# Kernel tuning notes

Hardware: AMD Instinct MI355X
Metric: run time of the kernel (lower is better)

The kernel has to match this reference:

```python
import jax, jax.numpy as jnp
import numpy as np
from jax import lax


def _conv(x, w, b):
    # NCHW valid conv, stride 1 (torch Conv2d semantics)
    y = lax.conv_general_dilated(x, w, (1, 1), 'VALID',
                                 dimension_numbers=('NCHW', 'OIHW', 'NCHW'))
    return y + b[None, :, None, None]


def _maxpool(x, k, s):
    return lax.reduce_window(x, -jnp.inf, lax.max, (1, 1, k, k), (1, 1, s, s), 'VALID')


def _lin(x, w, b):
    # torch nn.Linear: y = x @ W^T + b, applied to last dim
    return x @ w.T + b


def setup_inputs() -> dict:
    key = jax.random.key(0)
    ks = jax.random.split(key, 21)
    def f(i, shape, scale):
        return jax.random.normal(ks[i], shape, dtype=jnp.float32) * scale
    return {
        'x': f(0, (512, 1, 28, 28), 1.0),
        'c1_w': f(1, (50, 1, 3, 3), 0.33), 'c1_b': f(2, (50,), 0.1),
        'c2_w': f(3, (50, 50, 3, 3), 0.047), 'c2_b': f(4, (50,), 0.05),
        'c3_w': f(5, (50, 50, 3, 3), 0.047), 'c3_b': f(6, (50,), 0.05),
        'l1_w': f(7, (500, 50), 0.14), 'l1_b': f(8, (500,), 0.05),
        'l2_w': f(9, (10, 500), 0.045), 'l2_b': f(10, (10,), 0.05),
        'd1_w': f(11, (3, 8450), 0.011), 'd1_b': f(12, (3,), 0.05),
        'd2_w': f(13, (2, 1250), 0.028), 'd2_b': f(14, (2,), 0.05),
        'c1c3_w': f(15, (13, 13), 0.28), 'c1c3_b': f(16, (13,), 0.05),
        'c1l1_w': f(17, (500, 1), 1.0), 'c1l1_b': f(18, (500,), 0.05),
        'c2l1_w': f(19, (500, 5), 0.45), 'c2l1_b': f(20, (500,), 0.05),
    }


def reference(x, c1_w, c1_b, c2_w, c2_b, c3_w, c3_b, l1_w, l1_b, l2_w, l2_b,
              d1_w, d1_b, d2_w, d2_b, c1c3_w, c1c3_b, c1l1_w, c1l1_b,
              c2l1_w, c2l1_b):
    B = x.shape[0]
    # stage 1: conv1 + relu + pool2 -> [B,50,13,13]
    h1 = _maxpool(jax.nn.relu(_conv(x, c1_w, c1_b)), 2, 2)
    # router 1 (argmax over 3 branches): 0 -> conv2 path, 1 -> c1_c3 path, 2 -> early-exit linear path
    d1 = jnp.argmax(_lin(h1.reshape(B, -1), d1_w, d1_b), axis=1)  # [B]
    # branch l11 (d1==2): pool7 -> [B,50,1,1], Linear(1->500) on last dim -> [B,50,1,500]
    l11 = _lin(_maxpool(h1, 7, 7), c1l1_w, c1l1_b)
    # branch c3-direct (d1==1): Linear(13->13) on last dim, then conv3+relu+pool2 -> [B,50,5,5]
    c33 = _lin(h1, c1c3_w, c1c3_b)
    c3d = _maxpool(jax.nn.relu(_conv(c33, c3_w, c3_b)), 2, 2)
    # branch c2 (d1==0): conv2+relu+pool2 -> [B,50,5,5]
    h2 = _maxpool(jax.nn.relu(_conv(h1, c2_w, c2_b)), 2, 2)
    # router 2 (argmax over 2 sub-branches)
    d2 = jnp.argmax(_lin(h2.reshape(B, -1), d2_w, d2_b), axis=1)  # [B]
    # sub-branch c32 (d2==0): conv3+relu+pool2 -> [B,50,1,1]
    c32 = _maxpool(jax.nn.relu(_conv(h2, c3_w, c3_b)), 2, 2)
    # sub-branch l12 (d2==1): Linear(5->500) on last dim -> [B,50,5,500], pool3 -> [B,50,1,166]
    l12 = _maxpool(_lin(h2, c2l1_w, c2l1_b), 3, 3)

    def head(t):
        # original: .view(-1, 50) -> linear1/relu/linear2/log_softmax; row-major flatten per sample
        r = t.reshape(B, -1, 50)
        return jax.nn.log_softmax(_lin(jax.nn.relu(_lin(r, l1_w, l1_b)), l2_w, l2_b), axis=-1)

    dt = x.dtype
    m_l11 = (d1 == 2).astype(dt)[:, None, None]
    m_c3d = (d1 == 1).astype(dt)[:, None, None]
    m_c32 = ((d1 == 0) & (d2 == 0)).astype(dt)[:, None, None]
    m_l12 = ((d1 == 0) & (d2 == 1)).astype(dt)[:, None, None]
    # dense masked combine (static-shape equivalent of the gather/compute/concat dispatch);
    # branch order matches the original concatenation: l11, l12, c32, c3-direct
    out = jnp.concatenate([head(l11) * m_l11, head(l12) * m_l12,
                           head(c32) * m_c32, head(c3d) * m_c3d], axis=1)  # [B,692,10]
    return out, d1, d2
```

## Files before the change

### kernel.cpp

```cpp
#include <hip/hip_runtime.h>
#include <hip/hip_bf16.h>
#include <math.h>

#define BB 512
#define CC 50

typedef __attribute__((ext_vector_type(8))) __bf16 bf16x8;
typedef __attribute__((ext_vector_type(4))) float f32x4;

__global__ void k_zero(float* __restrict__ out, int n4) {
  int i = blockIdx.x * 256 + threadIdx.x;
  if (i < n4) {
    float4 z = {0.f, 0.f, 0.f, 0.f};
    ((float4*)out)[i] = z;
  }
}

__global__ void k_pack(const float* __restrict__ l1w, const float* __restrict__ l1b,
                       const float* __restrict__ l2w,
                       __bf16* __restrict__ W1p, float* __restrict__ W2t) {
  int idx = blockIdx.x * 256 + threadIdx.x;
  if (idx < 512 * 64) {
    int j = idx >> 6, k = idx & 63;
    float v = 0.f;
    if (j < 500) {
      if (k < 50) v = l1w[j * 50 + k];
      else if (k == 50) v = l1b[j];
    }
    W1p[idx] = (__bf16)v;
  } else if (idx < 512 * 64 + 512 * 12) {
    int i2 = idx - 512 * 64;
    int j = i2 / 12, n = i2 % 12;
    W2t[i2] = (n < 10 && j < 500) ? l2w[n * 500 + j] : 0.f;
  }
}

__global__ void k_conv1(const float* __restrict__ x, const float* __restrict__ w,
                        const float* __restrict__ bias, float* __restrict__ h1) {
  int idx = blockIdx.x * 256 + threadIdx.x;
  if (idx >= BB * CC * 169) return;
  int b = idx / (CC * 169);
  int rem = idx % (CC * 169);
  int c = rem / 169;
  int p = rem % 169;
  int py = p / 13, px = p % 13;
  const float* xi = x + b * 784;
  float wr[9];
#pragma unroll
  for (int i = 0; i < 9; i++) wr[i] = w[c * 9 + i];
  float m = -INFINITY;
#pragma unroll
  for (int dy = 0; dy < 2; dy++)
#pragma unroll
    for (int dx = 0; dx < 2; dx++) {
      int y0 = 2 * py + dy, x0 = 2 * px + dx;
      float s = 0.f;
#pragma unroll
      for (int ky = 0; ky < 3; ky++)
#pragma unroll
        for (int kx = 0; kx < 3; kx++)
          s += xi[(y0 + ky) * 28 + x0 + kx] * wr[ky * 3 + kx];
      m = fmaxf(m, s);
    }
  h1[idx] = fmaxf(m + bias[c], 0.f);
}

__global__ void k_d1p7(const float* __restrict__ h1, const float* __restrict__ w,
                       const float* __restrict__ bias, int* __restrict__ d1i,
                       float* __restrict__ outd1, float* __restrict__ p7) {
  int b = blockIdx.x, t = threadIdx.x;
  const float* hb = h1 + b * 8450;
  float s0 = 0.f, s1 = 0.f, s2 = 0.f;
  for (int i = t; i < 8450; i += 256) {
    float v = hb[i];
    s0 += v * w[i];
    s1 += v * w[8450 + i];
    s2 += v * w[16900 + i];
  }
#pragma unroll
  for (int off = 32; off >= 1; off >>= 1) {
    s0 += __shfl_down(s0, off);
    s1 += __shfl_down(s1, off);
    s2 += __shfl_down(s2, off);
  }
  __shared__ float red[4][3];
  if ((t & 63) == 0) { red[t >> 6][0] = s0; red[t >> 6][1] = s1; red[t >> 6][2] = s2; }
  __syncthreads();
  if (t == 0) {
    float l0 = bias[0], l1v = bias[1], l2v = bias[2];
    for (int wv = 0; wv < 4; wv++) { l0 += red[wv][0]; l1v += red[wv][1]; l2v += red[wv][2]; }
    int idx = 0; float best = l0;
    if (l1v > best) { best = l1v; idx = 1; }
    if (l2v > best) { best = l2v; idx = 2; }
    d1i[b] = idx;
    outd1[b] = (float)idx;
  }
  if (t < 50) {
    const float* hp = hb + t * 169;
    float m = -INFINITY;
#pragma unroll
    for (int y = 0; y < 7; y++)
#pragma unroll
      for (int x = 0; x < 7; x++) m = fmaxf(m, hp[y * 13 + x]);
    p7[b * 50 + t] = m;
  }
}

__global__ __launch_bounds__(256) void k_conv5m(
    const float* __restrict__ h1,
    const float* __restrict__ c2w, const float* __restrict__ c2b,
    const float* __restrict__ c3w, const float* __restrict__ c3b,
    const int* __restrict__ d1i,
    const float* __restrict__ w13, const float* __restrict__ b13,
    float* __restrict__ h2, float* __restrict__ c3d) {
  int id = blockIdx.x;
  int mode = id & 1, b = id >> 1;
  if (mode == 1 && d1i[b] != 1) return;
  __shared__ float sh[50 * 260];
  __shared__ float w13s[182];
  int t = threadIdx.x;
  for (int i = t; i < 8450; i += 256) {
    int ic = i / 169, r = i % 169;
    sh[ic * 260 + (r / 13) * 20 + (r % 13)] = h1[b * 8450 + i];
  }
  if (mode == 1) {
    for (int i = t; i < 182; i += 256) w13s[i] = (i < 169) ? w13[i] : b13[i - 169];
  }
  __syncthreads();
  if (mode == 1) {
    for (int p = t; p < 650; p += 256) {
      float* row = sh + (p / 13) * 260 + (p % 13) * 20;
      float r[13];
#pragma unroll
      for (int k = 0; k < 13; k++) r[k] = row[k];
#pragma unroll
      for (int xx = 0; xx < 13; xx++) {
        float s = w13s[169 + xx];
#pragma unroll
        for (int k = 0; k < 13; k++) s += r[k] * w13s[xx * 13 + k];
        row[xx] = s;
      }
    }
    __syncthreads();
  }
  if (t >= 250) return;
  int oc = t / 5, py = t % 5;
  const float* wb = (mode ? c3w : c2w) + oc * 450;
  float acc[5][4];
#pragma unroll
  for (int i = 0; i < 5; i++)
#pragma unroll
    for (int j = 0; j < 4; j++) acc[i][j] = 0.f;
  for (int ic = 0; ic < 50; ic++) {
    float wv[9];
#pragma unroll
    for (int i = 0; i < 9; i++) wv[i] = wb[ic * 9 + i];
    float r[4][13];
    const float* rp = sh + ic * 260 + 2 * py * 20;
#pragma unroll
    for (int rr = 0; rr < 4; rr++) {
      const float* p4 = rp + rr * 20;
      float4 q0 = *(const float4*)(p4);
      float4 q1 = *(const float4*)(p4 + 4);
      float4 q2 = *(const float4*)(p4 + 8);
      r[rr][0] = q0.x; r[rr][1] = q0.y; r[rr][2] = q0.z; r[rr][3] = q0.w;
      r[rr][4] = q1.x; r[rr][5] = q1.y; r[rr][6] = q1.z; r[rr][7] = q1.w;
      r[rr][8] = q2.x; r[rr][9] = q2.y; r[rr][10] = q2.z; r[rr][11] = q2.w;
      r[rr][12] = p4[12];
    }
#pragma unroll
    for (int px = 0; px < 5; px++)
#pragma unroll
      for (int dy = 0; dy < 2; dy++)
#pragma unroll
        for (int dx = 0; dx < 2; dx++) {
          float s = acc[px][dy * 2 + dx];
          int x0 = 2 * px + dx;
#pragma unroll
          for (int ky = 0; ky < 3; ky++)
#pragma unroll
            for (int kx = 0; kx < 3; kx++)
              s += r[dy + ky][x0 + kx] * wv[ky * 3 + kx];
          acc[px][dy * 2 + dx] = s;
        }
  }
  float bs = (mode ? c3b : c2b)[oc];
  float* outp = mode ? c3d : h2;
#pragma unroll
  for (int px = 0; px < 5; px++) {
    float m = fmaxf(fmaxf(acc[px][0], acc[px][1]), fmaxf(acc[px][2], acc[px][3]));
    outp[(b * 50 + oc) * 25 + py * 5 + px] = fmaxf(m + bs, 0.f);
  }
}

__global__ __launch_bounds__(256) void k_d2c(const float* __restrict__ h2,
                                             const float* __restrict__ d2w,
                                             const float* __restrict__ d2b,
                                             const float* __restrict__ c3w,
                                             const float* __restrict__ c3b,
                                             const float* __restrict__ c2l1w,
                                             const float* __restrict__ c2l1b,
                                             const int* __restrict__ d1i,
                                             int* __restrict__ d2i,
                                             float* __restrict__ outd2,
                                             float* __restrict__ c32,
                                             float* __restrict__ l12) {
  int b = blockIdx.x, t = threadIdx.x;
  __shared__ float hs[1250];
  __shared__ float wls[2500];
  __shared__ float bls[500];
  __shared__ float red[4][2];
  __shared__ int sd2;
  for (int i = t; i < 1250; i += 256) hs[i] = h2[b * 1250 + i];
  __syncthreads();
  float s0 = 0.f, s1 = 0.f;
  for (int i = t; i < 1250; i += 256) {
    float v = hs[i];
    s0 += v * d2w[i];
    s1 += v * d2w[1250 + i];
  }
#pragma unroll
  for (int off = 32; off >= 1; off >>= 1) {
    s0 += __shfl_down(s0, off);
    s1 += __shfl_down(s1, off);
  }
  if ((t & 63) == 0) { red[t >> 6][0] = s0; red[t >> 6][1] = s1; }
  __syncthreads();
  if (t == 0) {
    float l0 = d2b[0] + red[0][0] + red[1][0] + red[2][0] + red[3][0];
    float l1v = d2b[1] + red[0][1] + red[1][1] + red[2][1] + red[3][1];
    int idx = (l1v > l0) ? 1 : 0;
    d2i[b] = idx;
    outd2[b] = (float)idx;
    sd2 = idx;
  }
  __syncthreads();
  int d2v = sd2;
  if (d1i[b] != 0) return;
  if (d2v == 0) {
    if (t < 50) {
      const float* wb = c3w + t * 450;
      float a[4] = {0.f, 0.f, 0.f, 0.f};
      for (int ic = 0; ic < 50; ic++) {
        float r[4][4];
#pragma unroll
        for (int y = 0; y < 4; y++)
#pragma unroll
          for (int xx = 0; xx < 4; xx++) r[y][xx] = hs[ic * 25 + y * 5 + xx];
        float wv[9];
#pragma unroll
        for (int i = 0; i < 9; i++) wv[i] = wb[ic * 9 + i];
#pragma unroll
        for (int py = 0; py < 2; py++)
#pragma unroll
          for (int px = 0; px < 2; px++) {
            float s = a[py * 2 + px];
#pragma unroll
            for (int ky = 0; ky < 3; ky++)
#pragma unroll
              for (int kx = 0; kx < 3; kx++)
                s += r[py + ky][px + kx] * wv[ky * 3 + kx];
            a[py * 2 + px] = s;
          }
      }
      float m = fmaxf(fmaxf(a[0], a[1]), fmaxf(a[2], a[3]));
      c32[b * 50 + t] = fmaxf(m + c3b[t], 0.f);
    }
  } else {
    for (int i = t; i < 2500; i += 256) wls[i] = c2l1w[i];
    for (int i = t; i < 500; i += 256) bls[i] = c2l1b[i];
    __syncthreads();
    for (int o = t; o < 8300; o += 256) {
      int c = o / 166, tt = o % 166;
      const float* hb = hs + c * 25;
      float m = -INFINITY;
#pragma unroll
      for (int i = 0; i < 3; i++) {
        float a0 = hb[i * 5 + 0], a1 = hb[i * 5 + 1], a2 = hb[i * 5 + 2],
              a3 = hb[i * 5 + 3], a4 = hb[i * 5 + 4];
#pragma unroll
        for (int dj = 0; dj < 3; dj++) {
          int j = 3 * tt + dj;
          const float* wj = wls + j * 5;
          float s = bls[j] + a0 * wj[0] + a1 * wj[1] + a2 * wj[2] + a3 * wj[3] + a4 * wj[4];
          m = fmaxf(m, s);
        }
      }
      l12[b * 8300 + o] = m;
    }
  }
}

__global__ void k_count(const int* __restrict__ d1i, const int* __restrict__ d2i,
                        int* __restrict__ off, int* __restrict__ ntot) {
  __shared__ int s[512];
  int t = threadIdx.x;
  int d1 = d1i[t], d2 = d2i[t];
  int nr = (d1 == 2) ? 500 : (d1 == 1) ? 25 : (d2 == 1) ? 166 : 1;
  s[t] = nr;
  __syncthreads();
  for (int o = 1; o < 512; o <<= 1) {
    int v = (t >= o) ? s[t - o] : 0;
    __syncthreads();
    s[t] += v;
    __syncthreads();
  }
  off[t] = s[t] - nr;
  if (t == 511) ntot[0] = s[511];
}

__global__ void k_fill(const int* __restrict__ d1i, const int* __restrict__ d2i,
                       const int* __restrict__ off, int* __restrict__ rowtab) {
  int b = blockIdx.x;
  int d1 = d1i[b], d2 = d2i[b];
  int nr, rstart;
  if (d1 == 2)      { nr = 500; rstart = 0; }
  else if (d1 == 1) { nr = 25;  rstart = 667; }
  else if (d2 == 1) { nr = 166; rstart = 500; }
  else              { nr = 1;   rstart = 666; }
  int o = off[b];
  for (int i = threadIdx.x; i < nr; i += 256)
    rowtab[o + i] = (b << 10) | (rstart + i);
}

__device__ __forceinline__ int swz(int byteoff) {
  return byteoff ^ (((byteoff >> 7) & 7) << 4);
}

__global__ __launch_bounds__(256, 3) void k_headc(
    const float* __restrict__ c3d, const float* __restrict__ c32,
    const float* __restrict__ p7, const float* __restrict__ l12buf,
    const int* __restrict__ rowtab, const int* __restrict__ ntotp,
    const __bf16* __restrict__ W1p, const float* __restrict__ W2t,
    const float* __restrict__ l2b,
    const float* __restrict__ c1l1w, const float* __restrict__ c1l1b,
    float* __restrict__ out) {
  int ntot = ntotp[0];
  int blkbase = blockIdx.x * 64;
  if (blkbase >= ntot) return;

  __shared__ __align__(16) char wlds[16384];
  __shared__ __align__(16) float w2s[512 * 12];
  int t = threadIdx.x;
  int wv = t >> 6, lane = t & 63;
  int lr = lane & 15, lg = lane >> 4;

  for (int i = t; i < 1536; i += 256)
    ((float4*)w2s)[i] = ((const float4*)W2t)[i];

  int row = blkbase + wv * 16 + lr;
  int rowc = (row < ntot) ? row : (ntot - 1);
  int e = rowtab[rowc];
  int gb = e >> 10, orow = e & 1023;
  bf16x8 a1[2];
  {
    float pv = 0.f;
    const float* wsrc = nullptr;
    const float* bsrc = nullptr;
    const float* src = nullptr;
    bool isl11 = (orow < 500);
    if (isl11) {
      pv = p7[gb * 50 + orow / 10];
      int q = (orow % 10) * 50;
      wsrc = c1l1w + q;
      bsrc = c1l1b + q;
    } else if (orow < 666) {
      src = l12buf + gb * 8300 + (orow - 500) * 50;
    } else if (orow == 666) {
      src = c32 + gb * 50;
    } else {
      src = c3d + gb * 1250 + (orow - 667) * 50;
    }
#pragma unroll
    for (int ks = 0; ks < 2; ++ks) {
      float v[8];
      int k0 = ks * 32 + lg * 8;
      if (ks == 0 || lg < 2) {
        if (isl11) {
#pragma unroll
          for (int i = 0; i < 8; i += 2) {
            float2 wq = *(const float2*)(wsrc + k0 + i);
            float2 bq = *(const float2*)(bsrc + k0 + i);
            v[i] = pv * wq.x + bq.x;
            v[i + 1] = pv * wq.y + bq.y;
          }
        } else {
#pragma unroll
          for (int i = 0; i < 8; i += 2) {
            float2 q = *(const float2*)(src + k0 + i);
            v[i] = q.x; v[i + 1] = q.y;
          }
        }
      } else if (lg == 2) {
        float2 q;
        if (isl11) {
          float2 wq = *(const float2*)(wsrc + 48);
          float2 bq = *(const float2*)(bsrc + 48);
          q.x = pv * wq.x + bq.x; q.y = pv * wq.y + bq.y;
        } else {
          q = *(const float2*)(src + 48);
        }
        v[0] = q.x; v[1] = q.y; v[2] = 1.0f;
        v[3] = 0.f; v[4] = 0.f; v[5] = 0.f; v[6] = 0.f; v[7] = 0.f;
      } else {
#pragma unroll
        for (int i = 0; i < 8; ++i) v[i] = 0.f;
      }
      bf16x8 a;
#pragma unroll
      for (int i = 0; i < 8; ++i) a[i] = (__bf16)v[i];
      a1[ks] = a;
    }
  }

  float acc[4][10];
#pragma unroll
  for (int r = 0; r < 4; ++r)
#pragma unroll
    for (int n = 0; n < 10; ++n) acc[r][n] = 0.f;

  for (int p = 0; p < 4; ++p) {
    if (p > 0) __syncthreads();
    {
      const char* src = (const char*)W1p + p * 16384 + t * 64;
#pragma unroll
      for (int i = 0; i < 4; ++i) {
        float4 q = *(const float4*)(src + i * 16);
        *(float4*)(wlds + swz(t * 64 + i * 16)) = q;
      }
    }
    __syncthreads();
#pragma unroll
    for (int jl = 0; jl < 8; ++jl) {
      int jt = p * 8 + jl;
      int boff = jl * 2048 + lr * 128 + lg * 16;
      bf16x8 b0 = *(const bf16x8*)(wlds + swz(boff));
      bf16x8 b1 = *(const bf16x8*)(wlds + swz(boff + 64));
      const float* wr = w2s + (jt * 16 + lr) * 12;
      float4 w20 = *(const float4*)(wr);
      float4 w21 = *(const float4*)(wr + 4);
      float2 w22 = *(const float2*)(wr + 8);
      f32x4 h = {0.f, 0.f, 0.f, 0.f};
      h = __builtin_amdgcn_mfma_f32_16x16x32_bf16(a1[0], b0, h, 0, 0, 0);
      h = __builtin_amdgcn_mfma_f32_16x16x32_bf16(a1[1], b1, h, 0, 0, 0);
      float w2v[10] = {w20.x, w20.y, w20.z, w20.w, w21.x, w21.y, w21.z, w21.w, w22.x, w22.y};
#pragma unroll
      for (int r = 0; r < 4; ++r) {
        float hv = fmaxf(h[r], 0.f);
#pragma unroll
        for (int n = 0; n < 10; ++n) acc[r][n] += hv * w2v[n];
      }
    }
  }

#pragma unroll
  for (int r = 0; r < 4; ++r)
#pragma unroll
    for (int n = 0; n < 10; ++n) {
      float v = acc[r][n];
      v += __shfl_xor(v, 1);
      v += __shfl_xor(v, 2);
      v += __shfl_xor(v, 4);
      v += __shfl_xor(v, 8);
      acc[r][n] = v;
    }
  if (lr == 0) {
#pragma unroll
    for (int r = 0; r < 4; ++r) {
      int rw = blkbase + wv * 16 + lg * 4 + r;
      if (rw < ntot) {
        int e2 = rowtab[rw];
        int b2 = e2 >> 10, orow2 = e2 & 1023;
        float o[10];
        float m = -INFINITY;
#pragma unroll
        for (int n = 0; n < 10; ++n) {
          o[n] = acc[r][n] + l2b[n];
          m = fmaxf(m, o[n]);
        }
        float s = 0.f;
#pragma unroll
        for (int n = 0; n < 10; ++n) s += expf(o[n] - m);
        float lse = m + logf(s);
        float* orowp = out + (b2 * 692 + orow2) * 10;
#pragma unroll
        for (int n = 0; n < 10; ++n) orowp[n] = o[n] - lse;
      }
    }
  }
}

extern "C" void kernel_launch(void* const* d_in, const int* in_sizes, int n_in,
                              void* d_out, int out_size, void* d_ws, size_t ws_size,
                              hipStream_t stream) {
  const float* x     = (const float*)d_in[0];
  const float* c1w   = (const float*)d_in[1];
  const float* c1b   = (const float*)d_in[2];
  const float* c2w   = (const float*)d_in[3];
  const float* c2b   = (const float*)d_in[4];
  const float* c3w   = (const float*)d_in[5];
  const float* c3b   = (const float*)d_in[6];
  const float* l1w   = (const float*)d_in[7];
  const float* l1b   = (const float*)d_in[8];
  const float* l2w   = (const float*)d_in[9];
  const float* l2b   = (const float*)d_in[10];
  const float* d1w   = (const float*)d_in[11];
  const float* d1b   = (const float*)d_in[12];
  const float* d2w   = (const float*)d_in[13];
  const float* d2b   = (const float*)d_in[14];
  const float* c13w  = (const float*)d_in[15];
  const float* c13b  = (const float*)d_in[16];
  const float* c1l1w = (const float*)d_in[17];
  const float* c1l1b = (const float*)d_in[18];
  const float* c2l1w = (const float*)d_in[19];
  const float* c2l1b = (const float*)d_in[20];
  float* out = (float*)d_out;

  float* ws  = (float*)d_ws;
  float* h1  = ws;
  float* h2  = h1 + 4326400;
  float* c3d = h2 + 640000;
  float* c32 = c3d + 640000;
  float* p7  = c32 + 25600;
  int*   d1i = (int*)(p7 + 25600);
  int*   d2i = d1i + 512;
  __bf16* W1p = (__bf16*)(d2i + 512);
  float* W2t = (float*)(W1p + 512 * 64);
  int* off    = (int*)(W2t + 512 * 12);
  int* ntot   = off + 512;
  int* rowtab = ntot + 4;
  float* l12buf = h1;

  float* outd1 = out + 512 * 692 * 10;
  float* outd2 = outd1 + 512;

  k_zero<<<3460, 256, 0, stream>>>(out, 885510);
  k_pack<<<153, 256, 0, stream>>>(l1w, l1b, l2w, W1p, W2t);
  k_conv1<<<16900, 256, 0, stream>>>(x, c1w, c1b, h1);
  k_d1p7<<<512, 256, 0, stream>>>(h1, d1w, d1b, d1i, outd1, p7);
  k_conv5m<<<1024, 256, 0, stream>>>(h1, c2w, c2b, c3w, c3b, d1i,
                                     c13w, c13b, h2, c3d);
  k_d2c<<<512, 256, 0, stream>>>(h2, d2w, d2b, c3w, c3b, c2l1w, c2l1b,
                                 d1i, d2i, outd2, c32, l12buf);
  k_count<<<1, 512, 0, stream>>>(d1i, d2i, off, ntot);
  k_fill<<<512, 256, 0, stream>>>(d1i, d2i, off, rowtab);
  k_headc<<<4000, 256, 0, stream>>>(c3d, c32, p7, l12buf, rowtab, ntot,
                                    W1p, W2t, l2b, c1l1w, c1l1b, out);
}
```

Baseline: 220.7 us.

## Split conv5 input staging into two channel halves and compute two output channels per thread

```diff
diff --git a/kernel.cpp b/kernel.cpp
--- a/kernel.cpp
+++ b/kernel.cpp
@@ -116,80 +116,100 @@
   int id = blockIdx.x;
   int mode = id & 1, b = id >> 1;
   if (mode == 1 && d1i[b] != 1) return;
-  __shared__ float sh[50 * 260];
+  __shared__ float sh[25 * 260];
   __shared__ float w13s[182];
   int t = threadIdx.x;
-  for (int i = t; i < 8450; i += 256) {
-    int ic = i / 169, r = i % 169;
-    sh[ic * 260 + (r / 13) * 20 + (r % 13)] = h1[b * 8450 + i];
-  }
-  if (mode == 1) {
-    for (int i = t; i < 182; i += 256) w13s[i] = (i < 169) ? w13[i] : b13[i - 169];
-  }
-  __syncthreads();
-  if (mode == 1) {
-    for (int p = t; p < 650; p += 256) {
-      float* row = sh + (p / 13) * 260 + (p % 13) * 20;
-      float r[13];
-#pragma unroll
-      for (int k = 0; k < 13; k++) r[k] = row[k];
-#pragma unroll
-      for (int xx = 0; xx < 13; xx++) {
-        float s = w13s[169 + xx];
-#pragma unroll
-        for (int k = 0; k < 13; k++) s += r[k] * w13s[xx * 13 + k];
-        row[xx] = s;
-      }
+  int oc0 = (t / 5) * 2, py = t % 5;
+  const float* wall = mode ? c3w : c2w;
+  float acc[2][5][4];
+#pragma unroll
+  for (int u = 0; u < 2; u++)
+#pragma unroll
+    for (int i = 0; i < 5; i++)
+#pragma unroll
+      for (int j = 0; j < 4; j++) acc[u][i][j] = 0.f;
+
+  for (int half = 0; half < 2; ++half) {
+    if (half > 0) __syncthreads();
+    for (int i = t; i < 4225; i += 256) {
+      int ic = i / 169, r = i % 169;
+      sh[ic * 260 + (r / 13) * 20 + (r % 13)] = h1[b * 8450 + (half * 25 + ic) * 169 + r];
+    }
+    if (half == 0 && mode == 1) {
+      for (int i = t; i < 182; i += 256) w13s[i] = (i < 169) ? w13[i] : b13[i - 169];
     }
     __syncthreads();
-  }
-  if (t >= 250) return;
-  int oc = t / 5, py = t % 5;
-  const float* wb = (mode ? c3w : c2w) + oc * 450;
-  float acc[5][4];
-#pragma unroll
-  for (int i = 0; i < 5; i++)
-#pragma unroll
-    for (int j = 0; j < 4; j++) acc[i][j] = 0.f;
-  for (int ic = 0; ic < 50; ic++) {
-    float wv[9];
-#pragma unroll
-    for (int i = 0; i < 9; i++) wv[i] = wb[ic * 9 + i];
-    float r[4][13];
-    const float* rp = sh + ic * 260 + 2 * py * 20;
-#pragma unroll
-    for (int rr = 0; rr < 4; rr++) {
-      const float* p4 = rp + rr * 20;
-      float4 q0 = *(const float4*)(p4);
-      float4 q1 = *(const float4*)(p4 + 4);
-      float4 q2 = *(const float4*)(p4 + 8);
-      r[rr][0] = q0.x; r[rr][1] = q0.y; r[rr][2] = q0.z; r[rr][3] = q0.w;
-      r[rr][4] = q1.x; r[rr][5] = q1.y; r[rr][6] = q1.z; r[rr][7] = q1.w;
-      r[rr][8] = q2.x; r[rr][9] = q2.y; r[rr][10] = q2.z; r[rr][11] = q2.w;
-      r[rr][12] = p4[12];
-    }
-#pragma unroll
-    for (int px = 0; px < 5; px++)
-#pragma unroll
-      for (int dy = 0; dy < 2; dy++)
-#pragma unroll
-        for (int dx = 0; dx < 2; dx++) {
-          float s = acc[px][dy * 2 + dx];
-          int x0 = 2 * px + dx;
-#pragma unroll
-          for (int ky = 0; ky < 3; ky++)
-#pragma unroll
-            for (int kx = 0; kx < 3; kx++)
-              s += r[dy + ky][x0 + kx] * wv[ky * 3 + kx];
-          acc[px][dy * 2 + dx] = s;
-        }
-  }
-  float bs = (mode ? c3b : c2b)[oc];
+    if (mode == 1) {
+      for (int p = t; p < 325; p += 256) {
+        float* row = sh + (p / 13) * 260 + (p % 13) * 20;
+        float r[13];
+#pragma unroll
+        for (int k = 0; k < 13; k++) r[k] = row[k];
+#pragma unroll
+        for (int xx = 0; xx < 13; xx++) {
+          float s = w13s[169 + xx];
+#pragma unroll
+          for (int k = 0; k < 13; k++) s += r[k] * w13s[xx * 13 + k];
+          row[xx] = s;
+        }
+      }
+      __syncthreads();
+    }
+    if (t < 125) {
+      for (int icl = 0; icl < 25; ++icl) {
+        int icg = half * 25 + icl;
+        float wv0[9], wv1[9];
+#pragma unroll
+        for (int i = 0; i < 9; i++) wv0[i] = wall[oc0 * 450 + icg * 9 + i];
+#pragma unroll
+        for (int i = 0; i < 9; i++) wv1[i] = wall[(oc0 + 1) * 450 + icg * 9 + i];
+        float r[4][13];
+        const float* rp = sh + icl * 260 + 2 * py * 20;
+#pragma unroll
+        for (int rr = 0; rr < 4; rr++) {
+          const float* p4 = rp + rr * 20;
+          float4 q0 = *(const float4*)(p4);
+          float4 q1 = *(const float4*)(p4 + 4);
+          float4 q2 = *(const float4*)(p4 + 8);
+          r[rr][0] = q0.x; r[rr][1] = q0.y; r[rr][2] = q0.z; r[rr][3] = q0.w;
+          r[rr][4] = q1.x; r[rr][5] = q1.y; r[rr][6] = q1.z; r[rr][7] = q1.w;
+          r[rr][8] = q2.x; r[rr][9] = q2.y; r[rr][10] = q2.z; r[rr][11] = q2.w;
+          r[rr][12] = p4[12];
+        }
+#pragma unroll
+        for (int u = 0; u < 2; ++u) {
+          const float* wvu = u ? wv1 : wv0;
+#pragma unroll
+          for (int px = 0; px < 5; px++)
+#pragma unroll
+            for (int dy = 0; dy < 2; dy++)
+#pragma unroll
+              for (int dx = 0; dx < 2; dx++) {
+                float s = acc[u][px][dy * 2 + dx];
+                int x0 = 2 * px + dx;
+#pragma unroll
+                for (int ky = 0; ky < 3; ky++)
+#pragma unroll
+                  for (int kx = 0; kx < 3; kx++)
+                    s += r[dy + ky][x0 + kx] * wvu[ky * 3 + kx];
+                acc[u][px][dy * 2 + dx] = s;
+              }
+        }
+      }
+    }
+  }
+  if (t >= 125) return;
   float* outp = mode ? c3d : h2;
-#pragma unroll
-  for (int px = 0; px < 5; px++) {
-    float m = fmaxf(fmaxf(acc[px][0], acc[px][1]), fmaxf(acc[px][2], acc[px][3]));
-    outp[(b * 50 + oc) * 25 + py * 5 + px] = fmaxf(m + bs, 0.f);
+  const float* bp = mode ? c3b : c2b;
+#pragma unroll
+  for (int u = 0; u < 2; ++u) {
+    float bs = bp[oc0 + u];
+#pragma unroll
+    for (int px = 0; px < 5; px++) {
+      float m = fmaxf(fmaxf(acc[u][px][0], acc[u][px][1]),
+                      fmaxf(acc[u][px][2], acc[u][px][3]));
+      outp[(b * 50 + oc0 + u) * 25 + py * 5 + px] = fmaxf(m + bs, 0.f);
+    }
   }
 }
 
```

New measurement: 276.5 us. +25.3%, slower.
